# Kernel tuning notes

Measured on AMD Instinct MI355X. Metric: run time of the kernel, lower is better.

Reference implementation:

```python
import jax, jax.numpy as jnp
import numpy as np

N_EMBED = 1024
HEAD_SIZE = 128
B, T = 8, 2048


def setup_inputs() -> dict:
    key = jax.random.key(0)
    kx, kk, kq, kv = jax.random.split(key, 4)
    x = jax.random.normal(kx, (B, T, N_EMBED), dtype=jnp.float32)
    Wk = jax.random.normal(kk, (N_EMBED, HEAD_SIZE), dtype=jnp.float32) * (N_EMBED ** -0.5)
    Wq = jax.random.normal(kq, (N_EMBED, HEAD_SIZE), dtype=jnp.float32) * (N_EMBED ** -0.5)
    Wv = jax.random.normal(kv, (N_EMBED, HEAD_SIZE), dtype=jnp.float32) * (N_EMBED ** -0.5)
    return {"x": x, "Wk": Wk, "Wq": Wq, "Wv": Wv}


def reference(x, Wk, Wq, Wv):
    # x: [B, T, C]; single-head causal attention, dropout rate 0 (identity)
    t = x.shape[1]
    k = jnp.einsum("btc,ch->bth", x, Wk)  # keys
    q = jnp.einsum("btc,ch->bth", x, Wq)  # queries
    v = jnp.einsum("btc,ch->bth", x, Wv)  # values
    scale = k.shape[-1] ** -0.5
    scores = jnp.einsum("bqh,bkh->bqk", q, k) * scale  # [B, T, T]
    causal = jnp.tril(jnp.ones((t, t), dtype=bool))
    scores = jnp.where(causal, scores, -jnp.inf)
    attn = jax.nn.softmax(scores, axis=-1)
    return jnp.einsum("bqk,bkh->bqh", attn, v)
```

## Files before the change

kernel.cpp:

```cpp
#include <hip/hip_runtime.h>
#include <hip/hip_bf16.h>
#include <math.h>

#define B_ 8
#define T_ 2048
#define C_ 1024
#define D_ 128
#define M_ (B_*T_)

typedef __attribute__((ext_vector_type(8))) short short8;
typedef __attribute__((ext_vector_type(4))) float floatx4;
typedef __hip_bfloat16 bf16;

#define QSCALE 0.12751744416218247f

__global__ __launch_bounds__(256) void cvt_w3_kernel(const float* __restrict__ Wq,
                                                     const float* __restrict__ Wk,
                                                     const float* __restrict__ Wv,
                                                     bf16* __restrict__ Wt2) {
    __shared__ bf16 tl[64][136];
    const int t = threadIdx.x;
    const int kc = blockIdx.x, g = blockIdx.y;
    const int k0 = kc * 64;
    const float* W = (g == 0) ? Wq : (g == 1) ? Wk : Wv;
    {
        int k = t >> 2, n0 = (t & 3) * 32;
        const float* src = W + (size_t)(k0 + k) * 128 + n0;
#pragma unroll
        for (int j = 0; j < 4; ++j) {
            float4 v0 = *(const float4*)(src + j * 8);
            float4 v1 = *(const float4*)(src + j * 8 + 4);
            union { short8 s; __hip_bfloat162 h[4]; } u;
            __hip_bfloat162 h;
            h.x = __float2bfloat16(v0.x); h.y = __float2bfloat16(v0.y); u.h[0] = h;
            h.x = __float2bfloat16(v0.z); h.y = __float2bfloat16(v0.w); u.h[1] = h;
            h.x = __float2bfloat16(v1.x); h.y = __float2bfloat16(v1.y); u.h[2] = h;
            h.x = __float2bfloat16(v1.z); h.y = __float2bfloat16(v1.w); u.h[3] = h;
            *(short8*)&tl[k][n0 + j * 8] = u.s;
        }
    }
    __syncthreads();
    {
#pragma unroll
        for (int j = 0; j < 4; ++j) {
            int cid = t + j * 256;
            int lane = cid & 63, dk = (cid >> 6) & 1, cb = cid >> 7;
            int krow = dk * 32 + (lane >> 4) * 8;
            int ncol = cb * 16 + (lane & 15);
            union { short8 s; bf16 e[8]; } u;
#pragma unroll
            for (int e = 0; e < 8; ++e) u.e[e] = tl[krow + e][ncol];
            bf16* dst = Wt2 + ((((size_t)(g * 8 + cb) * 16 + kc) * 2 + dk) * 64 + lane) * 8;
            *(short8*)dst = u.s;
        }
    }
}

__global__ __launch_bounds__(512, 2) void proj10_kernel(const float* __restrict__ x,
                                                        const bf16* __restrict__ Wt2,
                                                        bf16* __restrict__ Qb,
                                                        bf16* __restrict__ Kb,
                                                        bf16* __restrict__ Vt) {
    __shared__ bf16 smem[2 * 64 * 72];
    const int t = threadIdx.x;
    const int wave = t >> 6, lane = t & 63;
    const int quad = lane >> 4, l15 = lane & 15;
    const int row0 = blockIdx.x * 64;
    const int xrow = t >> 3, xc8 = (t & 7) * 8;
    const float* xbase = x + (size_t)(row0 + xrow) * 1024 + xc8;
    const bf16* wbase = Wt2 + (size_t)lane * 8;

    floatx4 acc[4][3];
#pragma unroll
    for (int m = 0; m < 4; ++m)
#pragma unroll
        for (int n = 0; n < 3; ++n) acc[m][n] = (floatx4)0.0f;

    float4 xr0, xr1;
    short8 br[6];

    xr0 = *(const float4*)xbase;
    xr1 = *(const float4*)(xbase + 4);
    {
        union { short8 s; __hip_bfloat162 h[4]; } u;
        __hip_bfloat162 h;
        h.x = __float2bfloat16(xr0.x); h.y = __float2bfloat16(xr0.y); u.h[0] = h;
        h.x = __float2bfloat16(xr0.z); h.y = __float2bfloat16(xr0.w); u.h[1] = h;
        h.x = __float2bfloat16(xr1.x); h.y = __float2bfloat16(xr1.y); u.h[2] = h;
        h.x = __float2bfloat16(xr1.z); h.y = __float2bfloat16(xr1.w); u.h[3] = h;
        *(short8*)&smem[xrow * 72 + xc8] = u.s;
    }
    xr0 = *(const float4*)(xbase + 64);
    xr1 = *(const float4*)(xbase + 68);
#pragma unroll
    for (int n = 0; n < 3; ++n)
#pragma unroll
        for (int dk = 0; dk < 2; ++dk)
            br[dk * 3 + n] = *(const short8*)(wbase + ((size_t)((wave * 3 + n) * 16 + 0) * 1024 + dk * 512));

    for (int kc = 0; kc < 16; ++kc) {
        __syncthreads();
        short8 brn[6];
        if (kc < 15) {
#pragma unroll
            for (int n = 0; n < 3; ++n)
#pragma unroll
                for (int dk = 0; dk < 2; ++dk)
                    brn[dk * 3 + n] = *(const short8*)(wbase + ((size_t)((wave * 3 + n) * 16 + kc + 1) * 1024 + dk * 512));
            union { short8 s; __hip_bfloat162 h[4]; } u;
            __hip_bfloat162 h;
            h.x = __float2bfloat16(xr0.x); h.y = __float2bfloat16(xr0.y); u.h[0] = h;
            h.x = __float2bfloat16(xr0.z); h.y = __float2bfloat16(xr0.w); u.h[1] = h;
            h.x = __float2bfloat16(xr1.x); h.y = __float2bfloat16(xr1.y); u.h[2] = h;
            h.x = __float2bfloat16(xr1.z); h.y = __float2bfloat16(xr1.w); u.h[3] = h;
            *(short8*)&smem[((kc + 1) & 1) * 4608 + xrow * 72 + xc8] = u.s;
        }
        if (kc < 14) {
            const float* s = xbase + (kc + 2) * 64;
            xr0 = *(const float4*)s;
            xr1 = *(const float4*)(s + 4);
        }
        const bf16* lc = smem + (kc & 1) * 4608;
#pragma unroll
        for (int dk = 0; dk < 2; ++dk) {
            short8 af[4];
#pragma unroll
            for (int m = 0; m < 4; ++m)
                af[m] = *(const short8*)&lc[(m * 16 + l15) * 72 + dk * 32 + quad * 8];
#pragma unroll
            for (int m = 0; m < 4; ++m)
#pragma unroll
                for (int n = 0; n < 3; ++n)
                    acc[m][n] = __builtin_amdgcn_mfma_f32_16x16x32_bf16(af[m], br[dk * 3 + n], acc[m][n], 0, 0, 0);
        }
        if (kc < 15) {
#pragma unroll
            for (int i = 0; i < 6; ++i) br[i] = brn[i];
        }
    }

    __syncthreads();
    bf16* vtl = smem;
#pragma unroll
    for (int m = 0; m < 4; ++m)
#pragma unroll
        for (int r = 0; r < 4; ++r) {
            const int tt = m * 16 + quad * 4 + r;
            const int row = row0 + tt;
#pragma unroll
            for (int n = 0; n < 3; ++n) {
                const int colb = wave * 48 + n * 16;
                const int g = colb >> 7;
                const int lc_ = (colb & 127) + l15;
                const float v = acc[m][n][r];
                if (g == 0)      Qb[(size_t)row * 128 + lc_] = __float2bfloat16(v * QSCALE);
                else if (g == 1) Kb[(size_t)row * 128 + lc_] = __float2bfloat16(v);
                else             vtl[tt * 137 + lc_] = __float2bfloat16(v);
            }
        }
    __syncthreads();
    {
        int d = t >> 2, toff = (t & 3) * 16;
        union { short8 s[2]; bf16 e[16]; } u;
#pragma unroll
        for (int i = 0; i < 16; ++i) u.e[i] = vtl[(toff + i) * 137 + d];
        int bb = row0 >> 11, t0 = row0 & 2047;
        bf16* dst = Vt + (size_t)(bb * D_ + d) * T_ + t0 + toff;
        *(short8*)dst       = u.s[0];
        *(short8*)(dst + 8) = u.s[1];
    }
}

__global__ __launch_bounds__(256, 3) void flash_fm2_kernel(const bf16* __restrict__ Qb,
                                                           const bf16* __restrict__ Kb,
                                                           const bf16* __restrict__ Vt,
                                                           float* __restrict__ out,
                                                           bf16* __restrict__ Opart,
                                                           float* __restrict__ Lpart) {
    const int tile = blockIdx.x, seg = blockIdx.y, b = blockIdx.z;
    const int keys_total = (tile + 1) * 64;
    const int nseg = (keys_total + 255) >> 8;
    if (seg >= nseg) return;

    __shared__ bf16 lds_k[64][136];
    __shared__ bf16 lds_v[128][72];
    __shared__ bf16 lds_p[4][16][72];
    const int t = threadIdx.x;
    const int wave = t >> 6, lane = t & 63;
    const int quad = lane >> 4, l15 = lane & 15;
    const int q0 = tile * 64;
    const int k_start = seg << 8;
    const int k_end = min(k_start + 256, keys_total);
    const int nch = (k_end - k_start) >> 6;

    short8 qf[4];
    {
        int qm = q0 + wave * 16 + l15;
#pragma unroll
        for (int dk = 0; dk < 4; ++dk)
            qf[dk] = *(const short8*)(Qb + (size_t)(b * T_ + qm) * 128 + dk * 32 + quad * 8);
    }

    short8 kreg[4], vreg[4];
    {
        const int k0 = k_start;
#pragma unroll
        for (int j = 0; j < 4; ++j) {
            int c = t + j * 256;
            { int r = c >> 4, co = (c & 15) * 8;
              kreg[j] = *(const short8*)(Kb + (size_t)(b * T_ + k0 + r) * 128 + co); }
            { int d = c >> 3, co = (c & 7) * 8;
              vreg[j] = *(const short8*)(Vt + (size_t)b * (D_ * T_) + d * T_ + k0 + co); }
        }
    }

    floatx4 o_acc[8];
#pragma unroll
    for (int i = 0; i < 8; ++i) o_acc[i] = (floatx4)0.0f;
    float lp[4] = {0.f, 0.f, 0.f, 0.f};
    const int qrow = q0 + wave * 16 + quad * 4;

    for (int ch = 0; ch < nch; ++ch) {
        const int k0 = k_start + (ch << 6);
        __syncthreads();
#pragma unroll
        for (int j = 0; j < 4; ++j) {
            int c = t + j * 256;
            { int r = c >> 4, co = (c & 15) * 8; *(short8*)&lds_k[r][co] = kreg[j]; }
            { int d = c >> 3, co = (c & 7) * 8;  *(short8*)&lds_v[d][co] = vreg[j]; }
        }
        if (ch + 1 < nch) {
            const int kn = k0 + 64;
#pragma unroll
            for (int j = 0; j < 4; ++j) {
                int c = t + j * 256;
                { int r = c >> 4, co = (c & 15) * 8;
                  kreg[j] = *(const short8*)(Kb + (size_t)(b * T_ + kn + r) * 128 + co); }
                { int d = c >> 3, co = (c & 7) * 8;
                  vreg[j] = *(const short8*)(Vt + (size_t)b * (D_ * T_) + d * T_ + kn + co); }
            }
        }
        __syncthreads();

        floatx4 s[4];
#pragma unroll
        for (int nt = 0; nt < 4; ++nt) s[nt] = (floatx4)0.0f;
#pragma unroll
        for (int dk = 0; dk < 4; ++dk)
#pragma unroll
            for (int nt = 0; nt < 4; ++nt) {
                short8 kb = *(const short8*)&lds_k[nt * 16 + l15][dk * 32 + quad * 8];
                s[nt] = __builtin_amdgcn_mfma_f32_16x16x32_bf16(qf[dk], kb, s[nt], 0, 0, 0);
            }

        float sv[4][4];
#pragma unroll
        for (int nt = 0; nt < 4; ++nt)
#pragma unroll
            for (int r = 0; r < 4; ++r) sv[nt][r] = s[nt][r];

        if (k0 + 63 > q0) {
#pragma unroll
            for (int nt = 0; nt < 4; ++nt) {
                int key = k0 + nt * 16 + l15;
#pragma unroll
                for (int r = 0; r < 4; ++r)
                    if (key > qrow + r) sv[nt][r] = -1e30f;
            }
        }

#pragma unroll
        for (int nt = 0; nt < 4; ++nt)
#pragma unroll
            for (int r = 0; r < 4; ++r) sv[nt][r] = exp2f(sv[nt][r]);
#pragma unroll
        for (int r = 0; r < 4; ++r)
            lp[r] += (sv[0][r] + sv[1][r]) + (sv[2][r] + sv[3][r]);

#pragma unroll
        for (int nt = 0; nt < 4; ++nt)
#pragma unroll
            for (int r = 0; r < 4; ++r)
                lds_p[wave][quad * 4 + r][nt * 16 + l15] = __float2bfloat16(sv[nt][r]);
        short8 pa0 = *(const short8*)&lds_p[wave][l15][quad * 8];
        short8 pa1 = *(const short8*)&lds_p[wave][l15][32 + quad * 8];

#pragma unroll
        for (int nt = 0; nt < 8; ++nt) {
            short8 vb0 = *(const short8*)&lds_v[nt * 16 + l15][quad * 8];
            short8 vb1 = *(const short8*)&lds_v[nt * 16 + l15][32 + quad * 8];
            o_acc[nt] = __builtin_amdgcn_mfma_f32_16x16x32_bf16(pa0, vb0, o_acc[nt], 0, 0, 0);
            o_acc[nt] = __builtin_amdgcn_mfma_f32_16x16x32_bf16(pa1, vb1, o_acc[nt], 0, 0, 0);
        }
    }

    float l_i[4];
#pragma unroll
    for (int r = 0; r < 4; ++r) {
        float v = lp[r];
        v += __shfl_xor(v, 1);
        v += __shfl_xor(v, 2);
        v += __shfl_xor(v, 4);
        v += __shfl_xor(v, 8);
        l_i[r] = v;
    }

    const int lrow = wave * 16 + quad * 4;
    if (nseg == 1) {
        float inv_l[4];
#pragma unroll
        for (int r = 0; r < 4; ++r) inv_l[r] = 1.0f / l_i[r];
#pragma unroll
        for (int f = 0; f < 8; ++f)
#pragma unroll
            for (int r = 0; r < 4; ++r)
                out[(size_t)(b * T_ + qrow + r) * 128 + f * 16 + l15] = o_acc[f][r] * inv_l[r];
    } else {
        int pre = 0;
        for (int u = 4; u < tile; ++u) pre += (u + 4) >> 2;
        const size_t slot = (size_t)b * 140 + pre + seg;
        bf16* ob = Opart + slot * (64 * 128);
#pragma unroll
        for (int f = 0; f < 8; ++f)
#pragma unroll
            for (int r = 0; r < 4; ++r)
                ob[(size_t)(lrow + r) * 128 + f * 16 + l15] = __float2bfloat16(o_acc[f][r]);
        if (l15 == 0) {
#pragma unroll
            for (int r = 0; r < 4; ++r)
                Lpart[slot * 64 + lrow + r] = l_i[r];
        }
    }
}

__global__ __launch_bounds__(256) void combine4_kernel(const bf16* __restrict__ Opart,
                                                       const float* __restrict__ Lpart,
                                                       float* __restrict__ out) {
    const int tile = blockIdx.x + 4, b = blockIdx.y;
    const int nseg = (tile + 4) >> 2;
    int pre = 0;
    for (int u = 4; u < tile; ++u) pre += (u + 4) >> 2;
    const size_t slot0 = (size_t)b * 140 + pre;
    const int t = threadIdx.x;
    const int row = t >> 2, c0 = (t & 3) * 32;

    float lsum = 0.f;
    for (int j = 0; j < nseg; ++j) lsum += Lpart[(slot0 + j) * 64 + row];

    float acc[32];
#pragma unroll
    for (int i = 0; i < 32; ++i) acc[i] = 0.f;
    for (int j = 0; j < nseg; ++j) {
        const bf16* src = Opart + (slot0 + j) * (64 * 128) + (size_t)row * 128 + c0;
#pragma unroll
        for (int u = 0; u < 4; ++u) {
            short8 v8 = *(const short8*)(src + u * 8);
#pragma unroll
            for (int e = 0; e < 8; ++e) {
                union { unsigned int u32; float f; } cv;
                cv.u32 = ((unsigned int)(unsigned short)v8[e]) << 16;
                acc[u * 8 + e] += cv.f;
            }
        }
    }
    float inv = 1.0f / lsum;
    float* dst = out + (size_t)(b * T_ + tile * 64 + row) * 128 + c0;
#pragma unroll
    for (int i = 0; i < 32; ++i) dst[i] = acc[i] * inv;
}

extern "C" void kernel_launch(void* const* d_in, const int* in_sizes, int n_in,
                              void* d_out, int out_size, void* d_ws, size_t ws_size,
                              hipStream_t stream) {
    const float* x  = (const float*)d_in[0];
    const float* Wk = (const float*)d_in[1];
    const float* Wq = (const float*)d_in[2];
    const float* Wv = (const float*)d_in[3];
    float* out = (float*)d_out;

    char* ws = (char*)d_ws;
    bf16*  Wt2   = (bf16*)ws;
    bf16*  Qb    = (bf16*)(ws + 786432);
    bf16*  Kb    = (bf16*)(ws + 4980736);
    bf16*  Vt    = (bf16*)(ws + 9175040);
    bf16*  Opart = (bf16*)(ws + 13369344);
    float* Lpart = (float*)(ws + 31719424);

    cvt_w3_kernel<<<dim3(16, 3), 256, 0, stream>>>(Wq, Wk, Wv, Wt2);
    proj10_kernel<<<256, 512, 0, stream>>>(x, Wt2, Qb, Kb, Vt);
    flash_fm2_kernel<<<dim3(32, 8, B_), 256, 0, stream>>>(Qb, Kb, Vt, out, Opart, Lpart);
    combine4_kernel<<<dim3(28, B_), 256, 0, stream>>>(Opart, Lpart, out);
}
```

Measured before the change: 81.51 us.

## Warp-specialize QKV projection with producer waves issuing global-to-LDS loads

Rewrites the projection kernel so two producer waves stream x (fp32, XOR-swizzled) and weight tiles straight into double-buffered LDS via global_load_lds, while six consumer waves convert x to bf16 and run MFMAs on a 64x64 output tile each. The aim is to take global load latency and register staging off the compute waves and overlap loading with math. In exchange it uses 64KB of LDS, limits occupancy to one block per CU, and leaves a quarter of the waves doing no MFMA work. The fp32-to-bf16 conversion is now repeated by every consumer wave instead of being done once per element.

```diff
diff --git a/kernel.cpp b/kernel.cpp
--- a/kernel.cpp
+++ b/kernel.cpp
@@ -13,6 +13,10 @@
 typedef __hip_bfloat16 bf16;
 
 #define QSCALE 0.12751744416218247f
+
+#define GLDS16(gsrc, ldst) \
+    __builtin_amdgcn_global_load_lds((const __attribute__((address_space(1))) unsigned int*)(gsrc), \
+                                     (__attribute__((address_space(3))) unsigned int*)(ldst), 16, 0, 0)
 
 __global__ __launch_bounds__(256) void cvt_w3_kernel(const float* __restrict__ Wq,
                                                      const float* __restrict__ Wk,
@@ -56,108 +60,109 @@
     }
 }
 
-__global__ __launch_bounds__(512, 2) void proj10_kernel(const float* __restrict__ x,
+__global__ __launch_bounds__(512, 1) void proj16_kernel(const float* __restrict__ x,
                                                         const bf16* __restrict__ Wt2,
                                                         bf16* __restrict__ Qb,
                                                         bf16* __restrict__ Kb,
                                                         bf16* __restrict__ Vt) {
-    __shared__ bf16 smem[2 * 64 * 72];
+    __shared__ __attribute__((aligned(16))) char smem[65536];
     const int t = threadIdx.x;
     const int wave = t >> 6, lane = t & 63;
     const int quad = lane >> 4, l15 = lane & 15;
     const int row0 = blockIdx.x * 64;
-    const int xrow = t >> 3, xc8 = (t & 7) * 8;
-    const float* xbase = x + (size_t)(row0 + xrow) * 1024 + xc8;
-    const bf16* wbase = Wt2 + (size_t)lane * 8;
-
-    floatx4 acc[4][3];
-#pragma unroll
-    for (int m = 0; m < 4; ++m)
-#pragma unroll
-        for (int n = 0; n < 3; ++n) acc[m][n] = (floatx4)0.0f;
-
-    float4 xr0, xr1;
-    short8 br[6];
-
-    xr0 = *(const float4*)xbase;
-    xr1 = *(const float4*)(xbase + 4);
-    {
-        union { short8 s; __hip_bfloat162 h[4]; } u;
-        __hip_bfloat162 h;
-        h.x = __float2bfloat16(xr0.x); h.y = __float2bfloat16(xr0.y); u.h[0] = h;
-        h.x = __float2bfloat16(xr0.z); h.y = __float2bfloat16(xr0.w); u.h[1] = h;
-        h.x = __float2bfloat16(xr1.x); h.y = __float2bfloat16(xr1.y); u.h[2] = h;
-        h.x = __float2bfloat16(xr1.z); h.y = __float2bfloat16(xr1.w); u.h[3] = h;
-        *(short8*)&smem[xrow * 72 + xc8] = u.s;
-    }
-    xr0 = *(const float4*)(xbase + 64);
-    xr1 = *(const float4*)(xbase + 68);
-#pragma unroll
-    for (int n = 0; n < 3; ++n)
-#pragma unroll
-        for (int dk = 0; dk < 2; ++dk)
-            br[dk * 3 + n] = *(const short8*)(wbase + ((size_t)((wave * 3 + n) * 16 + 0) * 1024 + dk * 512));
-
-    for (int kc = 0; kc < 16; ++kc) {
-        __syncthreads();
-        short8 brn[6];
-        if (kc < 15) {
-#pragma unroll
-            for (int n = 0; n < 3; ++n)
-#pragma unroll
-                for (int dk = 0; dk < 2; ++dk)
-                    brn[dk * 3 + n] = *(const short8*)(wbase + ((size_t)((wave * 3 + n) * 16 + kc + 1) * 1024 + dk * 512));
-            union { short8 s; __hip_bfloat162 h[4]; } u;
-            __hip_bfloat162 h;
-            h.x = __float2bfloat16(xr0.x); h.y = __float2bfloat16(xr0.y); u.h[0] = h;
-            h.x = __float2bfloat16(xr0.z); h.y = __float2bfloat16(xr0.w); u.h[1] = h;
-            h.x = __float2bfloat16(xr1.x); h.y = __float2bfloat16(xr1.y); u.h[2] = h;
-            h.x = __float2bfloat16(xr1.z); h.y = __float2bfloat16(xr1.w); u.h[3] = h;
-            *(short8*)&smem[((kc + 1) & 1) * 4608 + xrow * 72 + xc8] = u.s;
-        }
-        if (kc < 14) {
-            const float* s = xbase + (kc + 2) * 64;
-            xr0 = *(const float4*)s;
-            xr1 = *(const float4*)(s + 4);
-        }
-        const bf16* lc = smem + (kc & 1) * 4608;
-#pragma unroll
-        for (int dk = 0; dk < 2; ++dk) {
-            short8 af[4];
+    bf16* vtl = (bf16*)smem;
+
+    if (wave >= 6) {
+        const int pw = wave - 6;
+        const float* xsrc[4];
+#pragma unroll
+        for (int j = 0; j < 4; ++j) {
+            const int i = pw * 4 + j;
+            xsrc[j] = x + (size_t)(row0 + i * 8 + (lane >> 3)) * 1024
+                        + ((lane & 7) ^ (lane >> 3)) * 4;
+        }
+#pragma unroll
+        for (int j = 0; j < 12; ++j) {
+            const int c = pw * 12 + j;
+            GLDS16(Wt2 + ((size_t)(c * 16 + 0) * 2 + 0) * 512 + lane * 8, smem + c * 1024);
+        }
+#pragma unroll
+        for (int j = 0; j < 4; ++j)
+            GLDS16(xsrc[j], smem + 49152 + (pw * 4 + j) * 1024);
+
+        for (int s = 0; s < 32; ++s) {
+            __syncthreads();
+            if (s < 31) {
+                const int sn = s + 1;
+                char* wd = smem + (sn & 1) * 24576;
+                char* xd = smem + 49152 + (sn & 1) * 8192;
+#pragma unroll
+                for (int j = 0; j < 12; ++j) {
+                    const int c = pw * 12 + j;
+                    GLDS16(Wt2 + ((size_t)(c * 16 + (sn >> 1)) * 2 + (sn & 1)) * 512 + lane * 8,
+                           wd + c * 1024);
+                }
+#pragma unroll
+                for (int j = 0; j < 4; ++j)
+                    GLDS16(xsrc[j] + sn * 32, xd + (pw * 4 + j) * 1024);
+            }
+        }
+    } else {
+        floatx4 acc[4][4];
+#pragma unroll
+        for (int m = 0; m < 4; ++m)
+#pragma unroll
+            for (int n = 0; n < 4; ++n) acc[m][n] = (floatx4)0.0f;
+
+        for (int s = 0; s < 32; ++s) {
+            __syncthreads();
+            const char* wb = smem + (s & 1) * 24576;
+            const char* xb = smem + 49152 + (s & 1) * 8192;
+            short8 af[4], bff[4];
+#pragma unroll
+            for (int m = 0; m < 4; ++m) {
+                const int r = m * 16 + l15;
+                const int r7 = r & 7;
+                float4 a0 = *(const float4*)(xb + r * 128 + (((2 * quad) ^ r7) * 16));
+                float4 a1 = *(const float4*)(xb + r * 128 + (((2 * quad + 1) ^ r7) * 16));
+                union { short8 s8; __hip_bfloat162 h[4]; } u;
+                __hip_bfloat162 h;
+                h.x = __float2bfloat16(a0.x); h.y = __float2bfloat16(a0.y); u.h[0] = h;
+                h.x = __float2bfloat16(a0.z); h.y = __float2bfloat16(a0.w); u.h[1] = h;
+                h.x = __float2bfloat16(a1.x); h.y = __float2bfloat16(a1.y); u.h[2] = h;
+                h.x = __float2bfloat16(a1.z); h.y = __float2bfloat16(a1.w); u.h[3] = h;
+                af[m] = u.s8;
+            }
+#pragma unroll
+            for (int n = 0; n < 4; ++n)
+                bff[n] = *(const short8*)(wb + (wave * 4 + n) * 1024 + lane * 16);
 #pragma unroll
             for (int m = 0; m < 4; ++m)
-                af[m] = *(const short8*)&lc[(m * 16 + l15) * 72 + dk * 32 + quad * 8];
-#pragma unroll
-            for (int m = 0; m < 4; ++m)
-#pragma unroll
-                for (int n = 0; n < 3; ++n)
-                    acc[m][n] = __builtin_amdgcn_mfma_f32_16x16x32_bf16(af[m], br[dk * 3 + n], acc[m][n], 0, 0, 0);
-        }
-        if (kc < 15) {
-#pragma unroll
-            for (int i = 0; i < 6; ++i) br[i] = brn[i];
-        }
-    }
-
-    __syncthreads();
-    bf16* vtl = smem;
-#pragma unroll
-    for (int m = 0; m < 4; ++m)
-#pragma unroll
-        for (int r = 0; r < 4; ++r) {
-            const int tt = m * 16 + quad * 4 + r;
-            const int row = row0 + tt;
-#pragma unroll
-            for (int n = 0; n < 3; ++n) {
-                const int colb = wave * 48 + n * 16;
-                const int g = colb >> 7;
-                const int lc_ = (colb & 127) + l15;
-                const float v = acc[m][n][r];
-                if (g == 0)      Qb[(size_t)row * 128 + lc_] = __float2bfloat16(v * QSCALE);
-                else if (g == 1) Kb[(size_t)row * 128 + lc_] = __float2bfloat16(v);
-                else             vtl[tt * 137 + lc_] = __float2bfloat16(v);
-            }
-        }
+#pragma unroll
+                for (int n = 0; n < 4; ++n)
+                    acc[m][n] = __builtin_amdgcn_mfma_f32_16x16x32_bf16(af[m], bff[n], acc[m][n], 0, 0, 0);
+        }
+
+#pragma unroll
+        for (int m = 0; m < 4; ++m)
+#pragma unroll
+            for (int r = 0; r < 4; ++r) {
+                const int tt = m * 16 + quad * 4 + r;
+                const int row = row0 + tt;
+#pragma unroll
+                for (int n = 0; n < 4; ++n) {
+                    const float v = acc[m][n][r];
+                    if (wave < 2) {
+                        Qb[(size_t)row * 128 + wave * 64 + n * 16 + l15] = __float2bfloat16(v * QSCALE);
+                    } else if (wave < 4) {
+                        Kb[(size_t)row * 128 + (wave - 2) * 64 + n * 16 + l15] = __float2bfloat16(v);
+                    } else {
+                        vtl[tt * 137 + (wave - 4) * 64 + n * 16 + l15] = __float2bfloat16(v);
+                    }
+                }
+            }
+    }
+
     __syncthreads();
     {
         int d = t >> 2, toff = (t & 3) * 16;
@@ -387,7 +392,7 @@
     float* Lpart = (float*)(ws + 31719424);
 
     cvt_w3_kernel<<<dim3(16, 3), 256, 0, stream>>>(Wq, Wk, Wv, Wt2);
-    proj10_kernel<<<256, 512, 0, stream>>>(x, Wt2, Qb, Kb, Vt);
+    proj16_kernel<<<256, 512, 0, stream>>>(x, Wt2, Qb, Kb, Vt);
     flash_fm2_kernel<<<dim3(32, 8, B_), 256, 0, stream>>>(Qb, Kb, Vt, out, Opart, Lpart);
     combine4_kernel<<<dim3(28, B_), 256, 0, stream>>>(Opart, Lpart, out);
 }
```

Measured after the change: 84.64 us. +3.8%, slower.
